# Kernel optimization log

Hardware: AMD Instinct MI355X
Metric: run time of the kernel (lower is better)

## Reference

```python
import jax, jax.numpy as jnp
import numpy as np

HIDDEN = 1024


def setup_inputs() -> dict:
    key = jax.random.key(0)
    ks = jax.random.split(key, 8)
    x_in, y_in, out_dim, hidden = 1024, 1024, 1024, HIDDEN
    Nx, Ny = 4096, 4096
    s = lambda d: 1.0 / np.sqrt(d)
    return {
        "x": jax.random.normal(ks[0], (Nx, x_in), jnp.float32),
        "y": jax.random.normal(ks[1], (Ny, y_in), jnp.float32),
        "Wq": jax.random.normal(ks[2], (hidden, x_in), jnp.float32) * s(x_in),
        "bq": jnp.zeros((hidden,), jnp.float32),
        "Wk": jax.random.normal(ks[3], (hidden, y_in), jnp.float32) * s(y_in),
        "bk": jnp.zeros((hidden,), jnp.float32),
        "Wv": jax.random.normal(ks[4], (out_dim, y_in), jnp.float32) * s(y_in),
        "bv": jnp.zeros((out_dim,), jnp.float32),
    }


def reference(x, y, Wq, bq, Wk, bk, Wv, bv):
    # Linear projections (torch Linear: x @ W.T + b)
    q = x @ Wq.T + bq          # [Nx, H]
    k = y @ Wk.T + bk          # [Ny, H]
    v = y @ Wv.T + bv          # [Ny, D_out]
    scores = (q @ k.T) / jnp.sqrt(jnp.asarray(HIDDEN, q.dtype))  # [Nx, Ny]
    attn = jax.nn.softmax(scores, axis=1)
    return attn @ v            # [Nx, D_out]
```

## Files before the change

### kernel.cpp

```cpp
#include <hip/hip_runtime.h>
#include <cstdint>
#include <cstddef>

typedef __attribute__((ext_vector_type(8))) __bf16 bf16x8;
typedef __attribute__((ext_vector_type(4))) float  f32x4;

__device__ __forceinline__ unsigned short f32_to_bf16(float f) {
    union { float f; unsigned int u; } cv;
    cv.f = f;
    unsigned int u = cv.u;
    return (unsigned short)((u + 0x7fffu + ((u >> 16) & 1u)) >> 16);
}

__device__ __forceinline__ void async_copy16(const unsigned short* g, unsigned short* lds) {
    __builtin_amdgcn_global_load_lds(
        (const __attribute__((address_space(1))) unsigned int*)g,
        (__attribute__((address_space(3))) unsigned int*)lds,
        16, 0, 0);
}

__global__ __launch_bounds__(256) void cast_all(
    const float* __restrict__ x,  const float* __restrict__ y,
    const float* __restrict__ wq, const float* __restrict__ wk, const float* __restrict__ wv,
    unsigned short* __restrict__ xb,  unsigned short* __restrict__ yb,
    unsigned short* __restrict__ wqb, unsigned short* __restrict__ wkb,
    unsigned short* __restrict__ wvb)
{
    int b = blockIdx.x;
    const float* s; unsigned short* d; int base;
    if      (b < 4096)  { s = x;  d = xb;  base = b; }
    else if (b < 8192)  { s = y;  d = yb;  base = b - 4096; }
    else if (b < 9216)  { s = wq; d = wqb; base = b - 8192; }
    else if (b < 10240) { s = wk; d = wkb; base = b - 9216; }
    else                { s = wv; d = wvb; base = b - 10240; }
    int i = base * 256 + threadIdx.x;
    float4 v = ((const float4*)s)[i];
    ushort4 o;
    o.x = f32_to_bf16(v.x);
    o.y = f32_to_bf16(v.y);
    o.z = f32_to_bf16(v.z);
    o.w = f32_to_bf16(v.w);
    ((ushort4*)d)[i] = o;
}

__device__ __forceinline__ void gemm_core64(
    const unsigned short* __restrict__ A, const unsigned short* __restrict__ B,
    int K, int rowBase, int colBase, int kBeg, int kEnd,
    unsigned short* ldsA, unsigned short* ldsB, f32x4 acc[4][4])
{
    const int tid  = threadIdx.x;
    const int lane = tid & 63;
    const int wave = tid >> 6;
    const int quad = lane >> 4;
    const int r    = lane & 15;
    const int wm   = wave >> 1;
    const int wn   = wave & 1;

    const int c1 = tid + 256;
    const long aOff0 = (long)(rowBase + (tid >> 2)) * K + (tid & 3) * 8;
    const long aOff1 = (long)(rowBase + (c1  >> 2)) * K + (c1  & 3) * 8;
    const long bOff0 = (long)(colBase + (tid >> 2)) * K + (tid & 3) * 8;
    const long bOff1 = (long)(colBase + (c1  >> 2)) * K + (c1  & 3) * 8;
    unsigned short* ldsA0 = ldsA + tid * 8;
    unsigned short* ldsA1 = ldsA + c1 * 8;
    unsigned short* ldsB0 = ldsB + tid * 8;
    unsigned short* ldsB1 = ldsB + c1 * 8;

    const int aReadOff = (wm * 64 + r) * 32 + quad * 8;
    const int bReadOff = (wn * 64 + r) * 32 + quad * 8;

    for (int k0 = kBeg; k0 < kEnd; k0 += 64) {
        __syncthreads();
        async_copy16(A + aOff0 + k0, ldsA0);
        async_copy16(A + aOff1 + k0, ldsA1);
        async_copy16(B + bOff0 + k0, ldsB0);
        async_copy16(B + bOff1 + k0, ldsB1);
        async_copy16(A + aOff0 + k0 + 32, ldsA0 + 4096);
        async_copy16(A + aOff1 + k0 + 32, ldsA1 + 4096);
        async_copy16(B + bOff0 + k0 + 32, ldsB0 + 4096);
        async_copy16(B + bOff1 + k0 + 32, ldsB1 + 4096);
        __builtin_amdgcn_s_waitcnt(0);
        __syncthreads();

#pragma unroll
        for (int h = 0; h < 2; ++h) {
            const unsigned short* a = ldsA + h * 4096;
            const unsigned short* b = ldsB + h * 4096;
            bf16x8 af[4], bfr[4];
#pragma unroll
            for (int i = 0; i < 4; ++i)
                af[i] = *(const bf16x8*)(a + aReadOff + i * 16 * 32);
#pragma unroll
            for (int j = 0; j < 4; ++j)
                bfr[j] = *(const bf16x8*)(b + bReadOff + j * 16 * 32);
#pragma unroll
            for (int i = 0; i < 4; ++i)
#pragma unroll
                for (int j = 0; j < 4; ++j)
                    acc[i][j] = __builtin_amdgcn_mfma_f32_16x16x32_bf16(af[i], bfr[j], acc[i][j], 0, 0, 0);
        }
    }
}

__global__ __launch_bounds__(256, 2)
void proj_batched(const unsigned short* __restrict__ xb, const unsigned short* __restrict__ yb,
                  const unsigned short* __restrict__ wqb, const unsigned short* __restrict__ wkb,
                  const unsigned short* __restrict__ wvb,
                  unsigned short* __restrict__ q, unsigned short* __restrict__ k,
                  unsigned short* __restrict__ vt,
                  const float* __restrict__ bq, const float* __restrict__ bk,
                  const float* __restrict__ bv)
{
    __shared__ __align__(16) unsigned short ldsA[128 * 64];
    __shared__ __align__(16) unsigned short ldsB[128 * 64];

    const int b = blockIdx.x;
    const int z = b >> 8;
    const int rb = b & 255;

    const unsigned short *A, *B;
    unsigned short* C;
    const float* bias;
    int N, rowBase, colBase;
    bool biasPerRow;
    if (z == 0) {
        A = xb; B = wqb; C = q; bias = bq; N = 1024; biasPerRow = false;
        colBase = (rb >> 5) * 128; rowBase = (rb & 31) * 128;
    } else if (z == 1) {
        A = yb; B = wkb; C = k; bias = bk; N = 1024; biasPerRow = false;
        colBase = (rb >> 5) * 128; rowBase = (rb & 31) * 128;
    } else {
        A = wvb; B = yb; C = vt; bias = bv; N = 4096; biasPerRow = true;
        colBase = (rb >> 3) * 128; rowBase = (rb & 7) * 128;
    }

    f32x4 acc[4][4];
#pragma unroll
    for (int i = 0; i < 4; ++i)
#pragma unroll
        for (int j = 0; j < 4; ++j)
            acc[i][j] = (f32x4){0.f, 0.f, 0.f, 0.f};

    gemm_core64(A, B, 1024, rowBase, colBase, 0, 1024, ldsA, ldsB, acc);

    const int lane = threadIdx.x & 63;
    const int wave = threadIdx.x >> 6;
    const int quad = lane >> 4;
    const int r    = lane & 15;
    const int orow0 = rowBase + (wave >> 1) * 64 + quad * 4;
    const int ocol0 = colBase + (wave & 1) * 64 + r;

#pragma unroll
    for (int i = 0; i < 4; ++i)
#pragma unroll
        for (int e = 0; e < 4; ++e) {
            const int row = orow0 + i * 16 + e;
            const float brow = biasPerRow ? bias[row] : 0.f;
#pragma unroll
            for (int j = 0; j < 4; ++j) {
                const int col = ocol0 + j * 16;
                const float bb = biasPerRow ? brow : bias[col];
                C[(long)row * N + col] = f32_to_bf16(acc[i][j][e] + bb);
            }
        }
}

__global__ __launch_bounds__(256, 2)
void scores_gemm(const unsigned short* __restrict__ q, const unsigned short* __restrict__ k,
                 unsigned short* __restrict__ P, float* __restrict__ lsum, float scale2)
{
    __shared__ __align__(16) unsigned short ldsA[128 * 64];
    __shared__ __align__(16) unsigned short ldsB[128 * 64];

    const int rowBase = blockIdx.y * 128;
    const int colBase = blockIdx.x * 128;

    f32x4 acc[4][4];
#pragma unroll
    for (int i = 0; i < 4; ++i)
#pragma unroll
        for (int j = 0; j < 4; ++j)
            acc[i][j] = (f32x4){0.f, 0.f, 0.f, 0.f};

    gemm_core64(q, k, 1024, rowBase, colBase, 0, 1024, ldsA, ldsB, acc);

    const int lane = threadIdx.x & 63;
    const int wave = threadIdx.x >> 6;
    const int quad = lane >> 4;
    const int r    = lane & 15;
    const int orow0 = rowBase + (wave >> 1) * 64 + quad * 4;
    const int ocol0 = colBase + (wave & 1) * 64 + r;

#pragma unroll
    for (int i = 0; i < 4; ++i)
#pragma unroll
        for (int e = 0; e < 4; ++e) {
            const int row = orow0 + i * 16 + e;
            float rs = 0.f;
#pragma unroll
            for (int j = 0; j < 4; ++j) {
                const int col = ocol0 + j * 16;
                const float p = exp2f(acc[i][j][e] * scale2);
                rs += p;
                P[(long)row * 4096 + col] = f32_to_bf16(p);
            }
#pragma unroll
            for (int m = 1; m < 16; m <<= 1) rs += __shfl_xor(rs, m, 64);
            if (r == 0) atomicAdd(&lsum[row], rs);
        }
}

__global__ __launch_bounds__(256, 2)
void out_gemm_splitk(const unsigned short* __restrict__ P, const unsigned short* __restrict__ vt,
                     float* __restrict__ O)
{
    __shared__ __align__(16) unsigned short ldsA[128 * 64];
    __shared__ __align__(16) unsigned short ldsB[128 * 64];

    const int bid = blockIdx.x;
    const int xt  = bid >> 7;
    const int yz  = bid & 127;
    const int yt  = yz >> 2;
    const int zt  = yz & 3;

    const int rowBase = yt * 128;
    const int colBase = xt * 128;
    const int kBeg = zt * 1024;

    f32x4 acc[4][4];
#pragma unroll
    for (int i = 0; i < 4; ++i)
#pragma unroll
        for (int j = 0; j < 4; ++j)
            acc[i][j] = (f32x4){0.f, 0.f, 0.f, 0.f};

    gemm_core64(P, vt, 4096, rowBase, colBase, kBeg, kBeg + 1024, ldsA, ldsB, acc);

    const int lane = threadIdx.x & 63;
    const int wave = threadIdx.x >> 6;
    const int quad = lane >> 4;
    const int r    = lane & 15;
    const int orow0 = rowBase + (wave >> 1) * 64 + quad * 4;
    const int ocol0 = colBase + (wave & 1) * 64 + r;

#pragma unroll
    for (int i = 0; i < 4; ++i)
#pragma unroll
        for (int e = 0; e < 4; ++e) {
            const int row = orow0 + i * 16 + e;
#pragma unroll
            for (int j = 0; j < 4; ++j) {
                const int col = ocol0 + j * 16;
                atomicAdd(&O[(long)row * 1024 + col], acc[i][j][e]);
            }
        }
}

__global__ __launch_bounds__(256) void norm_rows(float* __restrict__ O, const float* __restrict__ lsum) {
    int i = blockIdx.x * 256 + threadIdx.x;
    const float inv = 1.0f / lsum[i >> 8];
    float4 v = ((const float4*)O)[i];
    v.x *= inv; v.y *= inv; v.z *= inv; v.w *= inv;
    ((float4*)O)[i] = v;
}

extern "C" void kernel_launch(void* const* d_in, const int* in_sizes, int n_in,
                              void* d_out, int out_size, void* d_ws, size_t ws_size,
                              hipStream_t stream) {
    const float* x  = (const float*)d_in[0];
    const float* y  = (const float*)d_in[1];
    const float* Wq = (const float*)d_in[2];
    const float* bq = (const float*)d_in[3];
    const float* Wk = (const float*)d_in[4];
    const float* bk = (const float*)d_in[5];
    const float* Wv = (const float*)d_in[6];
    const float* bv = (const float*)d_in[7];

    constexpr int Nx = 4096, Ny = 4096, H = 1024, Dv = 1024, Kin = 1024;

    char* ws = (char*)d_ws;
    size_t off = 0;
    auto carve = [&](size_t bytes) {
        char* p = ws + off;
        off += (bytes + 255) & ~(size_t)255;
        return p;
    };

    unsigned short* q_bf  = (unsigned short*)carve((size_t)Nx * H * 2);
    unsigned short* k_bf  = (unsigned short*)carve((size_t)Ny * H * 2);
    unsigned short* vt_bf = (unsigned short*)carve((size_t)Dv * Ny * 2);
    float*          lsum  = (float*)carve((size_t)Nx * sizeof(float));

    char* overlay = ws + off;
    unsigned short* x_bf  = (unsigned short*)overlay;
    unsigned short* y_bf  = x_bf  + (size_t)Nx * Kin;
    unsigned short* Wq_bf = y_bf  + (size_t)Ny * Kin;
    unsigned short* Wk_bf = Wq_bf + (size_t)H  * Kin;
    unsigned short* Wv_bf = Wk_bf + (size_t)H  * Kin;
    unsigned short* P_bf  = (unsigned short*)overlay;

    hipMemsetAsync(lsum, 0, Nx * sizeof(float), stream);
    hipMemsetAsync(d_out, 0, (size_t)Nx * Dv * sizeof(float), stream);

    cast_all<<<11264, 256, 0, stream>>>(x, y, Wq, Wk, Wv, x_bf, y_bf, Wq_bf, Wk_bf, Wv_bf);

    proj_batched<<<768, 256, 0, stream>>>(x_bf, y_bf, Wq_bf, Wk_bf, Wv_bf,
                                          q_bf, k_bf, vt_bf, bq, bk, bv);

    const float scale2 = 1.4426950408889634f / 32.0f;
    scores_gemm<<<dim3(Ny / 128, Nx / 128), 256, 0, stream>>>(q_bf, k_bf, P_bf, lsum, scale2);

    out_gemm_splitk<<<1024, 256, 0, stream>>>(P_bf, vt_bf, (float*)d_out);

    norm_rows<<<Nx * Dv / 4 / 256, 256, 0, stream>>>((float*)d_out, lsum);
}
```

Before: 277.8 us.

## Double-buffer GEMM K-loop with prefetch and replace split-K atomics with partial buffers

```diff
diff --git a/kernel.cpp b/kernel.cpp
--- a/kernel.cpp
+++ b/kernel.cpp
@@ -43,7 +43,7 @@
     ((ushort4*)d)[i] = o;
 }
 
-__device__ __forceinline__ void gemm_core64(
+__device__ __forceinline__ void gemm_core_pf(
     const unsigned short* __restrict__ A, const unsigned short* __restrict__ B,
     int K, int rowBase, int colBase, int kBeg, int kEnd,
     unsigned short* ldsA, unsigned short* ldsB, f32x4 acc[4][4])
@@ -69,36 +69,37 @@
     const int aReadOff = (wm * 64 + r) * 32 + quad * 8;
     const int bReadOff = (wn * 64 + r) * 32 + quad * 8;
 
-    for (int k0 = kBeg; k0 < kEnd; k0 += 64) {
-        __syncthreads();
-        async_copy16(A + aOff0 + k0, ldsA0);
-        async_copy16(A + aOff1 + k0, ldsA1);
-        async_copy16(B + bOff0 + k0, ldsB0);
-        async_copy16(B + bOff1 + k0, ldsB1);
-        async_copy16(A + aOff0 + k0 + 32, ldsA0 + 4096);
-        async_copy16(A + aOff1 + k0 + 32, ldsA1 + 4096);
-        async_copy16(B + bOff0 + k0 + 32, ldsB0 + 4096);
-        async_copy16(B + bOff1 + k0 + 32, ldsB1 + 4096);
+    const int nSteps = (kEnd - kBeg) >> 5;
+
+    async_copy16(A + aOff0 + kBeg, ldsA0);
+    async_copy16(A + aOff1 + kBeg, ldsA1);
+    async_copy16(B + bOff0 + kBeg, ldsB0);
+    async_copy16(B + bOff1 + kBeg, ldsB1);
+
+    for (int s = 0; s < nSteps; ++s) {
+        const int cur = (s & 1) << 12;
+        const int nxt = cur ^ 4096;
         __builtin_amdgcn_s_waitcnt(0);
         __syncthreads();
-
-#pragma unroll
-        for (int h = 0; h < 2; ++h) {
-            const unsigned short* a = ldsA + h * 4096;
-            const unsigned short* b = ldsB + h * 4096;
-            bf16x8 af[4], bfr[4];
-#pragma unroll
-            for (int i = 0; i < 4; ++i)
-                af[i] = *(const bf16x8*)(a + aReadOff + i * 16 * 32);
+        if (s + 1 < nSteps) {
+            const int kn = kBeg + ((s + 1) << 5);
+            async_copy16(A + aOff0 + kn, ldsA0 + nxt);
+            async_copy16(A + aOff1 + kn, ldsA1 + nxt);
+            async_copy16(B + bOff0 + kn, ldsB0 + nxt);
+            async_copy16(B + bOff1 + kn, ldsB1 + nxt);
+        }
+        bf16x8 af[4], bfr[4];
+#pragma unroll
+        for (int i = 0; i < 4; ++i)
+            af[i] = *(const bf16x8*)(ldsA + cur + aReadOff + i * 16 * 32);
+#pragma unroll
+        for (int j = 0; j < 4; ++j)
+            bfr[j] = *(const bf16x8*)(ldsB + cur + bReadOff + j * 16 * 32);
+#pragma unroll
+        for (int i = 0; i < 4; ++i)
 #pragma unroll
             for (int j = 0; j < 4; ++j)
-                bfr[j] = *(const bf16x8*)(b + bReadOff + j * 16 * 32);
-#pragma unroll
-            for (int i = 0; i < 4; ++i)
-#pragma unroll
-                for (int j = 0; j < 4; ++j)
-                    acc[i][j] = __builtin_amdgcn_mfma_f32_16x16x32_bf16(af[i], bfr[j], acc[i][j], 0, 0, 0);
-        }
+                acc[i][j] = __builtin_amdgcn_mfma_f32_16x16x32_bf16(af[i], bfr[j], acc[i][j], 0, 0, 0);
     }
 }
 
@@ -111,8 +112,8 @@
                   const float* __restrict__ bq, const float* __restrict__ bk,
                   const float* __restrict__ bv)
 {
-    __shared__ __align__(16) unsigned short ldsA[128 * 64];
-    __shared__ __align__(16) unsigned short ldsB[128 * 64];
+    __shared__ __align__(16) unsigned short ldsA[2 * 128 * 32];
+    __shared__ __align__(16) unsigned short ldsB[2 * 128 * 32];
 
     const int b = blockIdx.x;
     const int z = b >> 8;
@@ -141,7 +142,7 @@
         for (int j = 0; j < 4; ++j)
             acc[i][j] = (f32x4){0.f, 0.f, 0.f, 0.f};
 
-    gemm_core64(A, B, 1024, rowBase, colBase, 0, 1024, ldsA, ldsB, acc);
+    gemm_core_pf(A, B, 1024, rowBase, colBase, 0, 1024, ldsA, ldsB, acc);
 
     const int lane = threadIdx.x & 63;
     const int wave = threadIdx.x >> 6;
@@ -169,8 +170,8 @@
 void scores_gemm(const unsigned short* __restrict__ q, const unsigned short* __restrict__ k,
                  unsigned short* __restrict__ P, float* __restrict__ lsum, float scale2)
 {
-    __shared__ __align__(16) unsigned short ldsA[128 * 64];
-    __shared__ __align__(16) unsigned short ldsB[128 * 64];
+    __shared__ __align__(16) unsigned short ldsA[2 * 128 * 32];
+    __shared__ __align__(16) unsigned short ldsB[2 * 128 * 32];
 
     const int rowBase = blockIdx.y * 128;
     const int colBase = blockIdx.x * 128;
@@ -182,7 +183,7 @@
         for (int j = 0; j < 4; ++j)
             acc[i][j] = (f32x4){0.f, 0.f, 0.f, 0.f};
 
-    gemm_core64(q, k, 1024, rowBase, colBase, 0, 1024, ldsA, ldsB, acc);
+    gemm_core_pf(q, k, 1024, rowBase, colBase, 0, 1024, ldsA, ldsB, acc);
 
     const int lane = threadIdx.x & 63;
     const int wave = threadIdx.x >> 6;
@@ -210,12 +211,13 @@
         }
 }
 
+template <int ATOMIC>
 __global__ __launch_bounds__(256, 2)
 void out_gemm_splitk(const unsigned short* __restrict__ P, const unsigned short* __restrict__ vt,
                      float* __restrict__ O)
 {
-    __shared__ __align__(16) unsigned short ldsA[128 * 64];
-    __shared__ __align__(16) unsigned short ldsB[128 * 64];
+    __shared__ __align__(16) unsigned short ldsA[2 * 128 * 32];
+    __shared__ __align__(16) unsigned short ldsB[2 * 128 * 32];
 
     const int bid = blockIdx.x;
     const int xt  = bid >> 7;
@@ -234,7 +236,7 @@
         for (int j = 0; j < 4; ++j)
             acc[i][j] = (f32x4){0.f, 0.f, 0.f, 0.f};
 
-    gemm_core64(P, vt, 4096, rowBase, colBase, kBeg, kBeg + 1024, ldsA, ldsB, acc);
+    gemm_core_pf(P, vt, 4096, rowBase, colBase, kBeg, kBeg + 1024, ldsA, ldsB, acc);
 
     const int lane = threadIdx.x & 63;
     const int wave = threadIdx.x >> 6;
@@ -243,6 +245,8 @@
     const int orow0 = rowBase + (wave >> 1) * 64 + quad * 4;
     const int ocol0 = colBase + (wave & 1) * 64 + r;
 
+    float* Odst = ATOMIC ? O : (O + (size_t)zt * (4096 * 1024));
+
 #pragma unroll
     for (int i = 0; i < 4; ++i)
 #pragma unroll
@@ -251,9 +255,28 @@
 #pragma unroll
             for (int j = 0; j < 4; ++j) {
                 const int col = ocol0 + j * 16;
-                atomicAdd(&O[(long)row * 1024 + col], acc[i][j][e]);
+                if (ATOMIC) atomicAdd(&Odst[(long)row * 1024 + col], acc[i][j][e]);
+                else        Odst[(long)row * 1024 + col] = acc[i][j][e];
             }
         }
+}
+
+__global__ __launch_bounds__(256) void reduce_norm(const float* __restrict__ parts,
+                                                   const float* __restrict__ lsum,
+                                                   float* __restrict__ O) {
+    const int i = blockIdx.x * 256 + threadIdx.x;
+    const float inv = 1.0f / lsum[i >> 8];
+    const size_t stride = (size_t)(4096 * 1024) / 4;
+    float4 a = ((const float4*)parts)[i];
+    float4 b = ((const float4*)parts)[i + stride];
+    float4 c = ((const float4*)parts)[i + 2 * stride];
+    float4 d = ((const float4*)parts)[i + 3 * stride];
+    float4 o;
+    o.x = (a.x + b.x + c.x + d.x) * inv;
+    o.y = (a.y + b.y + c.y + d.y) * inv;
+    o.z = (a.z + b.z + c.z + d.z) * inv;
+    o.w = (a.w + b.w + c.w + d.w) * inv;
+    ((float4*)O)[i] = o;
 }
 
 __global__ __launch_bounds__(256) void norm_rows(float* __restrict__ O, const float* __restrict__ lsum) {
@@ -299,8 +322,14 @@
     unsigned short* Wv_bf = Wk_bf + (size_t)H  * Kin;
     unsigned short* P_bf  = (unsigned short*)overlay;
 
+    const size_t overlay_bytes = (size_t)Nx * Ny * 2;
+    float* parts = (float*)(overlay + overlay_bytes);
+    const size_t need_parts = (overlay + overlay_bytes + 4 * (size_t)Nx * Dv * 4) - ws;
+    const bool useParts = ws_size >= need_parts;
+
     hipMemsetAsync(lsum, 0, Nx * sizeof(float), stream);
-    hipMemsetAsync(d_out, 0, (size_t)Nx * Dv * sizeof(float), stream);
+    if (!useParts)
+        hipMemsetAsync(d_out, 0, (size_t)Nx * Dv * sizeof(float), stream);
 
     cast_all<<<11264, 256, 0, stream>>>(x, y, Wq, Wk, Wv, x_bf, y_bf, Wq_bf, Wk_bf, Wv_bf);
 
@@ -310,7 +339,11 @@
     const float scale2 = 1.4426950408889634f / 32.0f;
     scores_gemm<<<dim3(Ny / 128, Nx / 128), 256, 0, stream>>>(q_bf, k_bf, P_bf, lsum, scale2);
 
-    out_gemm_splitk<<<1024, 256, 0, stream>>>(P_bf, vt_bf, (float*)d_out);
-
-    norm_rows<<<Nx * Dv / 4 / 256, 256, 0, stream>>>((float*)d_out, lsum);
-}
+    if (useParts) {
+        out_gemm_splitk<0><<<1024, 256, 0, stream>>>(P_bf, vt_bf, parts);
+        reduce_norm<<<Nx * Dv / 4 / 256, 256, 0, stream>>>(parts, lsum, (float*)d_out);
+    } else {
+        out_gemm_splitk<1><<<1024, 256, 0, stream>>>(P_bf, vt_bf, (float*)d_out);
+        norm_rows<<<Nx * Dv / 4 / 256, 256, 0, stream>>>((float*)d_out, lsum);
+    }
+}
```

Result: faster. 243.5 us (-12.4%).
